# Performance work log

Hardware: AMD Instinct MI355X
Metric: run time of the kernel (lower is better)

## Reference

```python
import jax, jax.numpy as jnp
import numpy as np


def setup_inputs() -> dict:
    key = jax.random.key(0)
    ks = jax.random.split(key, 6)
    B, S, E, H = 8, 2048, 1024, 64
    scale = 1.0 / np.sqrt(E)
    return {
        "query": jax.random.normal(ks[0], (B, S, E), dtype=jnp.float32),
        "key": jax.random.normal(ks[1], (B, S, E), dtype=jnp.float32),
        "value": jax.random.normal(ks[2], (B, S, E), dtype=jnp.float32),
        "Wq": jax.random.normal(ks[3], (E, H), dtype=jnp.float32) * scale,
        "bq": jnp.zeros((H,), dtype=jnp.float32),
        "Wk": jax.random.normal(ks[4], (E, H), dtype=jnp.float32) * scale,
        "bk": jnp.zeros((H,), dtype=jnp.float32),
        "Wv": jax.random.normal(ks[5], (E, H), dtype=jnp.float32) * scale,
        "bv": jnp.zeros((H,), dtype=jnp.float32),
    }


def reference(query, key, value, Wq, bq, Wk, bk, Wv, bv):
    # Linear projections: [B,S,E] @ [E,H] + [H] -> [B,S,H]
    q = jnp.einsum("bse,eh->bsh", query, Wq) + bq
    k = jnp.einsum("bse,eh->bsh", key, Wk) + bk
    v = jnp.einsum("bse,eh->bsh", value, Wv) + bv
    head_dim = q.shape[-1]
    # scores [B,S,S], softmax over last axis, then weighted sum of values
    scores = jnp.einsum("bqh,bkh->bqk", q, k) / jnp.sqrt(
        jnp.asarray(head_dim, dtype=q.dtype)
    )
    attn = jax.nn.softmax(scores, axis=-1)
    return jnp.einsum("bqk,bkh->bqh", attn, v)
```

## Files before the change

### kernel.cpp

```cpp
#include <hip/hip_runtime.h>
#include <math.h>

#define BB 8
#define SS 2048
#define EE 1024
#define HH 64
#define MM (BB * SS)

typedef unsigned short u16;
typedef __attribute__((ext_vector_type(8))) short short8;
typedef __attribute__((ext_vector_type(4))) float floatx4;

__device__ __forceinline__ u16 f2bf(float f) {
    union { float f; unsigned u; } a; a.f = f;
    unsigned r = a.u + 0x7fffu + ((a.u >> 16) & 1u);
    return (u16)(r >> 16);
}

__device__ __forceinline__ void split2(float f0, float f1, unsigned& hp, unsigned& lp) {
    union { float f; unsigned u; } a0, a1, h0, h1, l0, l1;
    a0.f = f0; a1.f = f1;
    h0.u = a0.u & 0xffff0000u;
    h1.u = a1.u & 0xffff0000u;
    l0.f = f0 - h0.f;
    l1.f = f1 - h1.f;
    hp = __builtin_amdgcn_perm(a1.u, a0.u, 0x07060302u);
    lp = __builtin_amdgcn_perm(l1.u, l0.u, 0x07060302u);
}

__device__ __forceinline__ void async_copy16(const u16* g, u16* l) {
    __builtin_amdgcn_global_load_lds(
        (const __attribute__((address_space(1))) unsigned*)g,
        (__attribute__((address_space(3))) unsigned*)l, 16, 0, 0);
}

template <int CTRL>
__device__ __forceinline__ float dppf(float x) {
    union { float f; int i; } a, b;
    a.f = x;
    b.i = __builtin_amdgcn_update_dpp(a.i, a.i, CTRL, 0xF, 0xF, true);
    return b.f;
}
__device__ __forceinline__ float red_max16(float x) {
    x = fmaxf(x, dppf<0xB1>(x));
    x = fmaxf(x, dppf<0x4E>(x));
    x = fmaxf(x, dppf<0x141>(x));
    x = fmaxf(x, dppf<0x140>(x));
    return x;
}
__device__ __forceinline__ float red_sum16(float x) {
    x += dppf<0xB1>(x);
    x += dppf<0x4E>(x);
    x += dppf<0x141>(x);
    x += dppf<0x140>(x);
    return x;
}

#define WP_MAT 131072

__global__ __launch_bounds__(512) void pack_w(
    const float* __restrict__ W0, const float* __restrict__ W1, const float* __restrict__ W2,
    u16* __restrict__ Wp)
{
    const int which = blockIdx.y;
    const float* __restrict__ W = (which == 0) ? W0 : (which == 1) ? W1 : W2;
    const float scale = (which == 0) ? 0.125f : 1.0f;
    const int t    = blockIdx.x;
    const int tid  = threadIdx.x;
    const int ks   = tid >> 8;
    const int nt   = (tid >> 6) & 3;
    const int lane = tid & 63;
    const int n    = lane & 15;
    const int g    = lane >> 4;

    const int k0 = t * 64 + ks * 32 + g * 8;
    const int c  = nt * 16 + n;

    float e[8];
    #pragma unroll
    for (int j = 0; j < 8; ++j) e[j] = W[(size_t)(k0 + j) * HH + c] * scale;

    unsigned hp[4], lp[4];
    #pragma unroll
    for (int i = 0; i < 4; ++i) split2(e[2 * i], e[2 * i + 1], hp[i], lp[i]);

    u16* dst = Wp + (size_t)which * WP_MAT
                  + ((size_t)(t * 8 + ks * 4 + nt) * 2) * 512 + lane * 8;
    *(uint4*)dst         = (uint4){hp[0], hp[1], hp[2], hp[3]};
    *(uint4*)(dst + 512) = (uint4){lp[0], lp[1], lp[2], lp[3]};
}

#define PCH 16

#define LOAD_A(AV, T)                                   \
    {                                                   \
        const float* p_ = ap + (T) * 64;                \
        AV[0] = *(const float4*)(p_ + 0);               \
        AV[1] = *(const float4*)(p_ + 4);               \
        AV[2] = *(const float4*)(p_ + 32);              \
        AV[3] = *(const float4*)(p_ + 36);              \
    }

#define VBAR4()                                                     \
    {                                                               \
        __builtin_amdgcn_sched_barrier(0);                          \
        asm volatile("s_waitcnt vmcnt(4)" ::: "memory");            \
        __builtin_amdgcn_s_barrier();                               \
        __builtin_amdgcn_sched_barrier(0);                          \
    }

#define PROJ_CHUNK(AV, CURBUF, TSTAGE, TPREF)                                      \
    {                                                                              \
        if ((TSTAGE) < PCH) {                                                      \
            const u16* src_ = wpb + (size_t)(TSTAGE) * 8192 + wave * 2048 + lane * 8; \
            u16* dst_ = &Wb[(CURBUF) ^ 1][wave * 2048];                            \
            async_copy16(src_ + 0 * 512, dst_ + 0 * 512);                          \
            async_copy16(src_ + 1 * 512, dst_ + 1 * 512);                          \
            async_copy16(src_ + 2 * 512, dst_ + 2 * 512);                          \
            async_copy16(src_ + 3 * 512, dst_ + 3 * 512);                          \
        }                                                                          \
        __builtin_amdgcn_sched_barrier(0);                                         \
        short8 ah0, ah1, al0, al1;                                                 \
        {                                                                          \
            unsigned hp0, lp0, hp1, lp1, hp2, lp2, hp3, lp3;                       \
            split2(AV[0].x, AV[0].y, hp0, lp0);                                    \
            split2(AV[0].z, AV[0].w, hp1, lp1);                                    \
            split2(AV[1].x, AV[1].y, hp2, lp2);                                    \
            split2(AV[1].z, AV[1].w, hp3, lp3);                                    \
            union { uint4 u; short8 s; } ch_, cl_;                                 \
            ch_.u = (uint4){hp0, hp1, hp2, hp3};                                   \
            cl_.u = (uint4){lp0, lp1, lp2, lp3};                                   \
            ah0 = ch_.s; al0 = cl_.s;                                              \
            split2(AV[2].x, AV[2].y, hp0, lp0);                                    \
            split2(AV[2].z, AV[2].w, hp1, lp1);                                    \
            split2(AV[3].x, AV[3].y, hp2, lp2);                                    \
            split2(AV[3].z, AV[3].w, hp3, lp3);                                    \
            ch_.u = (uint4){hp0, hp1, hp2, hp3};                                   \
            cl_.u = (uint4){lp0, lp1, lp2, lp3};                                   \
            ah1 = ch_.s; al1 = cl_.s;                                              \
        }                                                                          \
        if ((TPREF) < PCH) LOAD_A(AV, TPREF);                                      \
        _Pragma("unroll")                                                          \
        for (int nt = 0; nt < 4; ++nt) {                                           \
            const short8 whf = *(const short8*)&Wb[CURBUF][nt * 1024 + lane * 8];  \
            const short8 wlf = *(const short8*)&Wb[CURBUF][nt * 1024 + 512 + lane * 8]; \
            acc[nt] = __builtin_amdgcn_mfma_f32_16x16x32_bf16(ah0, whf, acc[nt], 0, 0, 0); \
            acc[nt] = __builtin_amdgcn_mfma_f32_16x16x32_bf16(al0, whf, acc[nt], 0, 0, 0); \
            acc[nt] = __builtin_amdgcn_mfma_f32_16x16x32_bf16(ah0, wlf, acc[nt], 0, 0, 0); \
        }                                                                          \
        _Pragma("unroll")                                                          \
        for (int nt = 0; nt < 4; ++nt) {                                           \
            const short8 whf = *(const short8*)&Wb[CURBUF][4096 + nt * 1024 + lane * 8]; \
            const short8 wlf = *(const short8*)&Wb[CURBUF][4096 + nt * 1024 + 512 + lane * 8]; \
            acc[nt] = __builtin_amdgcn_mfma_f32_16x16x32_bf16(ah1, whf, acc[nt], 0, 0, 0); \
            acc[nt] = __builtin_amdgcn_mfma_f32_16x16x32_bf16(al1, whf, acc[nt], 0, 0, 0); \
            acc[nt] = __builtin_amdgcn_mfma_f32_16x16x32_bf16(ah1, wlf, acc[nt], 0, 0, 0); \
        }                                                                          \
    }

__global__ __launch_bounds__(256) void proj_mfma(
    const float* __restrict__ A0, const float* __restrict__ A1, const float* __restrict__ A2,
    const u16* __restrict__ Wp,
    const float* __restrict__ b0, const float* __restrict__ b1, const float* __restrict__ b2,
    u16* __restrict__ o0, u16* __restrict__ o1, u16* __restrict__ o2)
{
    const int which = blockIdx.y;
    const float* __restrict__ A    = (which == 0) ? A0 : (which == 1) ? A1 : A2;
    const float* __restrict__ bias = (which == 0) ? b0 : (which == 1) ? b1 : b2;
    u16* __restrict__ out          = (which == 0) ? o0 : (which == 1) ? o1 : o2;
    const float bscale = (which == 0) ? 0.125f : 1.0f;

    __shared__ __align__(16) u16 Wb[2][8192];

    const int tid  = threadIdx.x;
    const int lane = tid & 63;
    const int wave = tid >> 6;
    const int n    = lane & 15;
    const int g    = lane >> 4;
    const int row0 = blockIdx.x * 64;

    const float* __restrict__ ap = A + (size_t)(row0 + wave * 16 + n) * EE + g * 8;
    const u16* __restrict__ wpb = Wp + (size_t)which * WP_MAT;

    floatx4 acc[4];
    #pragma unroll
    for (int nt = 0; nt < 4; ++nt) acc[nt] = (floatx4){0.f, 0.f, 0.f, 0.f};

    float4 avA[4], avB[4];
    LOAD_A(avA, 0);
    LOAD_A(avB, 1);
    {
        const u16* src = wpb + wave * 2048 + lane * 8;
        u16* dst = &Wb[0][wave * 2048];
        #pragma unroll
        for (int i = 0; i < 4; ++i)
            async_copy16(src + i * 512, dst + i * 512);
    }
    __syncthreads();

    for (int tt = 0; tt < 12; tt += 2) {
        PROJ_CHUNK(avA, 0, tt + 1, tt + 2);
        VBAR4();
        PROJ_CHUNK(avB, 1, tt + 2, tt + 3);
        VBAR4();
    }
    PROJ_CHUNK(avA, 0, 13, 14);  VBAR4();
    PROJ_CHUNK(avB, 1, 14, 15);  VBAR4();
    PROJ_CHUNK(avA, 0, 15, 16);  __syncthreads();
    PROJ_CHUNK(avB, 1, 16, 17);

    #pragma unroll
    for (int nt = 0; nt < 4; ++nt) {
        const float bv = bias[nt * 16 + n] * bscale;
        #pragma unroll
        for (int r = 0; r < 4; ++r) {
            const int row = row0 + wave * 16 + g * 4 + r;
            out[(size_t)row * HH + nt * 16 + n] = f2bf(acc[nt][r] + bv);
        }
    }
}

__global__ __launch_bounds__(256) void flash_mfma(
    const u16* __restrict__ qp, const u16* __restrict__ kp,
    const u16* __restrict__ vp, float* __restrict__ out)
{
    __shared__ __align__(16) u16 Ks[2][64 * 64];
    __shared__ __align__(16) u16 Vt[2][64 * 64];
    __shared__ __align__(16) u16 Pw[4][16 * 72];

    const int b    = blockIdx.y;
    const int q0   = blockIdx.x * 32;
    const int tid  = threadIdx.x;
    const int lane = tid & 63;
    const int wave = tid >> 6;
    const int wq   = wave & 1;
    const int ks   = wave >> 1;
    const int n    = lane & 15;
    const int g    = lane >> 4;

    const u16* qrow = qp + ((size_t)b * SS + q0 + wq * 16 + n) * HH;
    const short8 qa0 = *(const short8*)(qrow + g * 8);
    const short8 qa1 = *(const short8*)(qrow + 32 + g * 8);

    floatx4 Oa[4];
    #pragma unroll
    for (int ht = 0; ht < 4; ++ht) Oa[ht] = (floatx4){0.f, 0.f, 0.f, 0.f};
    float m_i[4], l_ln[4];
    #pragma unroll
    for (int r = 0; r < 4; ++r) { m_i[r] = -1e30f; l_ln[r] = 0.f; }

    const u16* kb = kp + (size_t)b * SS * HH;
    const u16* vb = vp + (size_t)b * SS * HH;

    const int jK0 = tid >> 3, jK1 = 32 + (tid >> 3), cs = tid & 7;
    const int jV  = (tid & 15) * 4, hV = (tid >> 4) * 4;

    short8  kr0, kr1;
    ushort4 vr0, vr1, vr2, vr3;

    kr0 = *(const short8*)(kb + (size_t)jK0 * HH + cs * 8);
    kr1 = *(const short8*)(kb + (size_t)jK1 * HH + cs * 8);
    vr0 = *(const ushort4*)(vb + (size_t)(jV + 0) * HH + hV);
    vr1 = *(const ushort4*)(vb + (size_t)(jV + 1) * HH + hV);
    vr2 = *(const ushort4*)(vb + (size_t)(jV + 2) * HH + hV);
    vr3 = *(const ushort4*)(vb + (size_t)(jV + 3) * HH + hV);
    {
        *(short8*)&Ks[0][jK0 * 64 + ((cs ^ (jK0 & 7)) << 3)] = kr0;
        *(short8*)&Ks[0][jK1 * 64 + ((cs ^ (jK1 & 7)) << 3)] = kr1;
        const u16* a0 = (const u16*)&vr0; const u16* a1 = (const u16*)&vr1;
        const u16* a2 = (const u16*)&vr2; const u16* a3 = (const u16*)&vr3;
        #pragma unroll
        for (int i = 0; i < 4; ++i) {
            const int h = hV + i;
            ushort4 w; w.x = a0[i]; w.y = a1[i]; w.z = a2[i]; w.w = a3[i];
            *(ushort4*)((char*)&Vt[0][0] + h * 128 + (((jV >> 3) ^ (h & 7)) << 4) + ((jV & 4) << 1)) = w;
        }
    }
    __syncthreads();

    for (int t = 0; t < SS / 64; ++t) {
        const int cur = t & 1;

        if (t + 1 < SS / 64) {
            const size_t kt = (size_t)(t + 1) * 64;
            kr0 = *(const short8*)(kb + (kt + jK0) * HH + cs * 8);
            kr1 = *(const short8*)(kb + (kt + jK1) * HH + cs * 8);
            vr0 = *(const ushort4*)(vb + (kt + jV + 0) * HH + hV);
            vr1 = *(const ushort4*)(vb + (kt + jV + 1) * HH + hV);
            vr2 = *(const ushort4*)(vb + (kt + jV + 2) * HH + hV);
            vr3 = *(const ushort4*)(vb + (kt + jV + 3) * HH + hV);
        }

        floatx4 S[2];
        #pragma unroll
        for (int nt = 0; nt < 2; ++nt) {
            const int j = ks * 32 + nt * 16 + n;
            const short8 kf0 = *(const short8*)&Ks[cur][j * 64 + (((0 + g) ^ (j & 7)) << 3)];
            const short8 kf1 = *(const short8*)&Ks[cur][j * 64 + (((4 + g) ^ (j & 7)) << 3)];
            floatx4 a = (floatx4){0.f, 0.f, 0.f, 0.f};
            __builtin_amdgcn_s_setprio(1);
            a = __builtin_amdgcn_mfma_f32_16x16x32_bf16(qa0, kf0, a, 0, 0, 0);
            a = __builtin_amdgcn_mfma_f32_16x16x32_bf16(qa1, kf1, a, 0, 0, 0);
            __builtin_amdgcn_s_setprio(0);
            S[nt] = a;
        }

        float mx[4];
        #pragma unroll
        for (int r = 0; r < 4; ++r)
            mx[r] = red_max16(fmaxf(S[0][r], S[1][r]));

        float alpha[4];
        #pragma unroll
        for (int r = 0; r < 4; ++r) {
            const float Mn = fmaxf(m_i[r], mx[r]);
            alpha[r] = __expf(m_i[r] - Mn);
            m_i[r]   = Mn;
        }
        float p[2][4];
        #pragma unroll
        for (int nt = 0; nt < 2; ++nt)
            #pragma unroll
            for (int r = 0; r < 4; ++r)
                p[nt][r] = __expf(S[nt][r] - m_i[r]);
        #pragma unroll
        for (int r = 0; r < 4; ++r)
            l_ln[r] = l_ln[r] * alpha[r] + (p[0][r] + p[1][r]);
        #pragma unroll
        for (int ht = 0; ht < 4; ++ht)
            #pragma unroll
            for (int r = 0; r < 4; ++r) Oa[ht][r] *= alpha[r];

        #pragma unroll
        for (int nt = 0; nt < 2; ++nt)
            #pragma unroll
            for (int r = 0; r < 4; ++r)
                Pw[wave][(g * 4 + r) * 72 + nt * 16 + n] = f2bf(p[nt][r]);
        const short8 pa = *(const short8*)&Pw[wave][n * 72 + g * 8];

        __builtin_amdgcn_s_setprio(1);
        #pragma unroll
        for (int ht = 0; ht < 4; ++ht) {
            const int h = ht * 16 + n;
            const short8 vf = *(const short8*)((const char*)&Vt[cur][0] + h * 128 +
                                               ((((ks << 2) + g) ^ (h & 7)) << 4));
            Oa[ht] = __builtin_amdgcn_mfma_f32_16x16x32_bf16(pa, vf, Oa[ht], 0, 0, 0);
        }
        __builtin_amdgcn_s_setprio(0);

        if (t + 1 < SS / 64) {
            const int nx = cur ^ 1;
            *(short8*)&Ks[nx][jK0 * 64 + ((cs ^ (jK0 & 7)) << 3)] = kr0;
            *(short8*)&Ks[nx][jK1 * 64 + ((cs ^ (jK1 & 7)) << 3)] = kr1;
            const u16* a0 = (const u16*)&vr0; const u16* a1 = (const u16*)&vr1;
            const u16* a2 = (const u16*)&vr2; const u16* a3 = (const u16*)&vr3;
            #pragma unroll
            for (int i = 0; i < 4; ++i) {
                const int h = hV + i;
                ushort4 w; w.x = a0[i]; w.y = a1[i]; w.z = a2[i]; w.w = a3[i];
                *(ushort4*)((char*)&Vt[nx][0] + h * 128 + (((jV >> 3) ^ (h & 7)) << 4) + ((jV & 4) << 1)) = w;
            }
        }
        __syncthreads();
    }

    float l_i[4];
    #pragma unroll
    for (int r = 0; r < 4; ++r) l_i[r] = red_sum16(l_ln[r]);

    float* Cb = (float*)&Ks[0][0];
    float* Cm = Cb + 2 * 16 * 68;
    float* Cl = Cm + 32;
    if (ks == 1) {
        #pragma unroll
        for (int ht = 0; ht < 4; ++ht)
            #pragma unroll
            for (int r = 0; r < 4; ++r)
                Cb[(wq * 16 + g * 4 + r) * 68 + ht * 16 + n] = Oa[ht][r];
        if (n == 0)
            #pragma unroll
            for (int r = 0; r < 4; ++r) {
                Cm[wq * 16 + g * 4 + r] = m_i[r];
                Cl[wq * 16 + g * 4 + r] = l_i[r];
            }
    }
    __syncthreads();
    if (ks == 0) {
        float a0v[4], a1v[4], linv[4];
        #pragma unroll
        for (int r = 0; r < 4; ++r) {
            const int m = g * 4 + r;
            const float m1 = Cm[wq * 16 + m], l1 = Cl[wq * 16 + m];
            const float M  = fmaxf(m_i[r], m1);
            const float e0 = __expf(m_i[r] - M), e1 = __expf(m1 - M);
            a0v[r] = e0; a1v[r] = e1;
            linv[r] = 1.f / (l_i[r] * e0 + l1 * e1);
        }
        #pragma unroll
        for (int ht = 0; ht < 4; ++ht)
            #pragma unroll
            for (int r = 0; r < 4; ++r) {
                const float o1 = Cb[(wq * 16 + g * 4 + r) * 68 + ht * 16 + n];
                const float v  = (Oa[ht][r] * a0v[r] + o1 * a1v[r]) * linv[r];
                out[((size_t)b * SS + q0 + wq * 16 + g * 4 + r) * HH + ht * 16 + n] = v;
            }
    }
}

extern "C" void kernel_launch(void* const* d_in, const int* in_sizes, int n_in,
                              void* d_out, int out_size, void* d_ws, size_t ws_size,
                              hipStream_t stream) {
    const float* query = (const float*)d_in[0];
    const float* key   = (const float*)d_in[1];
    const float* value = (const float*)d_in[2];
    const float* Wq    = (const float*)d_in[3];
    const float* bq    = (const float*)d_in[4];
    const float* Wk    = (const float*)d_in[5];
    const float* bk    = (const float*)d_in[6];
    const float* Wv    = (const float*)d_in[7];
    const float* bv    = (const float*)d_in[8];
    float* out = (float*)d_out;

    u16* qp = (u16*)d_ws;
    u16* kp = qp + (size_t)MM * HH;
    u16* vp = kp + (size_t)MM * HH;
    u16* Wp = vp + (size_t)MM * HH;

    dim3 wgrid(EE / 64, 3);
    pack_w<<<wgrid, 512, 0, stream>>>(Wq, Wk, Wv, Wp);

    dim3 pgrid(MM / 64, 3);
    proj_mfma<<<pgrid, 256, 0, stream>>>(query, key, value,
                                         Wp,
                                         bq, bk, bv,
                                         qp, kp, vp);

    dim3 agrid(SS / 32, BB);
    flash_mfma<<<agrid, 256, 0, stream>>>(qp, kp, vp, out);
}
```

Baseline: 260.0 us.

## Widen flash block to 8 waves over 128-key tiles with single-buffered LDS

The attention kernel now runs 512 threads per block and processes 128 keys per iteration, splitting the key dimension across four wave groups instead of two. The shared K/V tiles become single-buffered, with an extra barrier before writing the next tile. The final merge combines four partial softmax states per query row instead of two. The aim is more parallel work per block and fewer loop iterations. The cost is that the double-buffer overlap is lost, an extra sync is added per iteration, and the merge epilogue is heavier.

Result: no change. 261.5 us (+0.6%).

```diff
diff --git a/kernel.cpp b/kernel.cpp
--- a/kernel.cpp
+++ b/kernel.cpp
@@ -220,13 +220,43 @@
     }
 }
 
-__global__ __launch_bounds__(256) void flash_mfma(
+#define KVB 128
+#define NIT (SS / KVB)
+
+#define WRITE_KV()                                                              \
+    {                                                                           \
+        *(short8*)&Ks[jK * 64 + ((cs2 ^ (jK & 7)) << 3)]       = kr0;           \
+        *(short8*)&Ks[jK * 64 + (((cs2 + 1) ^ (jK & 7)) << 3)] = kr1;           \
+        const u16* a0 = (const u16*)&vr0; const u16* a1 = (const u16*)&vr1;     \
+        const u16* a2 = (const u16*)&vr2; const u16* a3 = (const u16*)&vr3;     \
+        _Pragma("unroll")                                                       \
+        for (int i = 0; i < 4; ++i) {                                           \
+            const int h = hV + i;                                               \
+            ushort4 w; w.x = a0[i]; w.y = a1[i]; w.z = a2[i]; w.w = a3[i];      \
+            *(ushort4*)((char*)Vt + h * 256 + (((jV >> 3) ^ (h & 7)) << 4)      \
+                        + ((jV & 4) << 1)) = w;                                 \
+        }                                                                       \
+    }
+
+#define LOAD_KV(T)                                                              \
+    {                                                                           \
+        const size_t kt = (size_t)(T) * KVB;                                    \
+        kr0 = *(const short8*)(kb + (kt + jK) * HH + cs2 * 8);                  \
+        kr1 = *(const short8*)(kb + (kt + jK) * HH + cs2 * 8 + 8);              \
+        vr0 = *(const ushort4*)(vb + (kt + jV + 0) * HH + hV);                  \
+        vr1 = *(const ushort4*)(vb + (kt + jV + 1) * HH + hV);                  \
+        vr2 = *(const ushort4*)(vb + (kt + jV + 2) * HH + hV);                  \
+        vr3 = *(const ushort4*)(vb + (kt + jV + 3) * HH + hV);                  \
+    }
+
+__global__ __launch_bounds__(512) void flash_mfma(
     const u16* __restrict__ qp, const u16* __restrict__ kp,
     const u16* __restrict__ vp, float* __restrict__ out)
 {
-    __shared__ __align__(16) u16 Ks[2][64 * 64];
-    __shared__ __align__(16) u16 Vt[2][64 * 64];
-    __shared__ __align__(16) u16 Pw[4][16 * 72];
+    __shared__ __align__(16) u16 SM[25600];
+    u16* Ks = SM;
+    u16* Vt = SM + 8192;
+    u16* Pw = SM + 16384;
 
     const int b    = blockIdx.y;
     const int q0   = blockIdx.x * 32;
@@ -252,51 +282,27 @@
     const u16* kb = kp + (size_t)b * SS * HH;
     const u16* vb = vp + (size_t)b * SS * HH;
 
-    const int jK0 = tid >> 3, jK1 = 32 + (tid >> 3), cs = tid & 7;
-    const int jV  = (tid & 15) * 4, hV = (tid >> 4) * 4;
+    const int jK  = tid >> 2;
+    const int cs2 = (tid & 3) * 2;
+    const int jV  = (tid & 31) * 4;
+    const int hV  = (tid >> 5) * 4;
 
     short8  kr0, kr1;
     ushort4 vr0, vr1, vr2, vr3;
 
-    kr0 = *(const short8*)(kb + (size_t)jK0 * HH + cs * 8);
-    kr1 = *(const short8*)(kb + (size_t)jK1 * HH + cs * 8);
-    vr0 = *(const ushort4*)(vb + (size_t)(jV + 0) * HH + hV);
-    vr1 = *(const ushort4*)(vb + (size_t)(jV + 1) * HH + hV);
-    vr2 = *(const ushort4*)(vb + (size_t)(jV + 2) * HH + hV);
-    vr3 = *(const ushort4*)(vb + (size_t)(jV + 3) * HH + hV);
-    {
-        *(short8*)&Ks[0][jK0 * 64 + ((cs ^ (jK0 & 7)) << 3)] = kr0;
-        *(short8*)&Ks[0][jK1 * 64 + ((cs ^ (jK1 & 7)) << 3)] = kr1;
-        const u16* a0 = (const u16*)&vr0; const u16* a1 = (const u16*)&vr1;
-        const u16* a2 = (const u16*)&vr2; const u16* a3 = (const u16*)&vr3;
-        #pragma unroll
-        for (int i = 0; i < 4; ++i) {
-            const int h = hV + i;
-            ushort4 w; w.x = a0[i]; w.y = a1[i]; w.z = a2[i]; w.w = a3[i];
-            *(ushort4*)((char*)&Vt[0][0] + h * 128 + (((jV >> 3) ^ (h & 7)) << 4) + ((jV & 4) << 1)) = w;
-        }
-    }
+    LOAD_KV(0);
+    WRITE_KV();
     __syncthreads();
 
-    for (int t = 0; t < SS / 64; ++t) {
-        const int cur = t & 1;
-
-        if (t + 1 < SS / 64) {
-            const size_t kt = (size_t)(t + 1) * 64;
-            kr0 = *(const short8*)(kb + (kt + jK0) * HH + cs * 8);
-            kr1 = *(const short8*)(kb + (kt + jK1) * HH + cs * 8);
-            vr0 = *(const ushort4*)(vb + (kt + jV + 0) * HH + hV);
-            vr1 = *(const ushort4*)(vb + (kt + jV + 1) * HH + hV);
-            vr2 = *(const ushort4*)(vb + (kt + jV + 2) * HH + hV);
-            vr3 = *(const ushort4*)(vb + (kt + jV + 3) * HH + hV);
-        }
+    for (int t = 0; t < NIT; ++t) {
+        if (t + 1 < NIT) LOAD_KV(t + 1);
 
         floatx4 S[2];
         #pragma unroll
         for (int nt = 0; nt < 2; ++nt) {
             const int j = ks * 32 + nt * 16 + n;
-            const short8 kf0 = *(const short8*)&Ks[cur][j * 64 + (((0 + g) ^ (j & 7)) << 3)];
-            const short8 kf1 = *(const short8*)&Ks[cur][j * 64 + (((4 + g) ^ (j & 7)) << 3)];
+            const short8 kf0 = *(const short8*)&Ks[j * 64 + (((0 + g) ^ (j & 7)) << 3)];
+            const short8 kf1 = *(const short8*)&Ks[j * 64 + (((4 + g) ^ (j & 7)) << 3)];
             floatx4 a = (floatx4){0.f, 0.f, 0.f, 0.f};
             __builtin_amdgcn_s_setprio(1);
             a = __builtin_amdgcn_mfma_f32_16x16x32_bf16(qa0, kf0, a, 0, 0, 0);
@@ -335,74 +341,75 @@
         for (int nt = 0; nt < 2; ++nt)
             #pragma unroll
             for (int r = 0; r < 4; ++r)
-                Pw[wave][(g * 4 + r) * 72 + nt * 16 + n] = f2bf(p[nt][r]);
-        const short8 pa = *(const short8*)&Pw[wave][n * 72 + g * 8];
+                Pw[wave * 1152 + (g * 4 + r) * 72 + nt * 16 + n] = f2bf(p[nt][r]);
+        const short8 pa = *(const short8*)&Pw[wave * 1152 + n * 72 + g * 8];
 
         __builtin_amdgcn_s_setprio(1);
         #pragma unroll
         for (int ht = 0; ht < 4; ++ht) {
             const int h = ht * 16 + n;
-            const short8 vf = *(const short8*)((const char*)&Vt[cur][0] + h * 128 +
+            const short8 vf = *(const short8*)((const char*)Vt + h * 256 +
                                                ((((ks << 2) + g) ^ (h & 7)) << 4));
             Oa[ht] = __builtin_amdgcn_mfma_f32_16x16x32_bf16(pa, vf, Oa[ht], 0, 0, 0);
         }
         __builtin_amdgcn_s_setprio(0);
 
-        if (t + 1 < SS / 64) {
-            const int nx = cur ^ 1;
-            *(short8*)&Ks[nx][jK0 * 64 + ((cs ^ (jK0 & 7)) << 3)] = kr0;
-            *(short8*)&Ks[nx][jK1 * 64 + ((cs ^ (jK1 & 7)) << 3)] = kr1;
-            const u16* a0 = (const u16*)&vr0; const u16* a1 = (const u16*)&vr1;
-            const u16* a2 = (const u16*)&vr2; const u16* a3 = (const u16*)&vr3;
-            #pragma unroll
-            for (int i = 0; i < 4; ++i) {
-                const int h = hV + i;
-                ushort4 w; w.x = a0[i]; w.y = a1[i]; w.z = a2[i]; w.w = a3[i];
-                *(ushort4*)((char*)&Vt[nx][0] + h * 128 + (((jV >> 3) ^ (h & 7)) << 4) + ((jV & 4) << 1)) = w;
-            }
-        }
         __syncthreads();
+        if (t + 1 < NIT) WRITE_KV();
+        __syncthreads();
     }
 
     float l_i[4];
     #pragma unroll
     for (int r = 0; r < 4; ++r) l_i[r] = red_sum16(l_ln[r]);
 
-    float* Cb = (float*)&Ks[0][0];
-    float* Cm = Cb + 2 * 16 * 68;
-    float* Cl = Cm + 32;
-    if (ks == 1) {
+    float* Cb = (float*)SM;
+    float* Cm = Cb + 3 * 2 * 16 * 68;
+    float* Cl = Cm + 96;
+
+    if (ks != 0) {
+        float* dst = Cb + ((ks - 1) * 2 + wq) * 16 * 68;
         #pragma unroll
         for (int ht = 0; ht < 4; ++ht)
             #pragma unroll
             for (int r = 0; r < 4; ++r)
-                Cb[(wq * 16 + g * 4 + r) * 68 + ht * 16 + n] = Oa[ht][r];
+                dst[(g * 4 + r) * 68 + ht * 16 + n] = Oa[ht][r];
         if (n == 0)
             #pragma unroll
             for (int r = 0; r < 4; ++r) {
-                Cm[wq * 16 + g * 4 + r] = m_i[r];
-                Cl[wq * 16 + g * 4 + r] = l_i[r];
+                Cm[((ks - 1) * 2 + wq) * 16 + g * 4 + r] = m_i[r];
+                Cl[((ks - 1) * 2 + wq) * 16 + g * 4 + r] = l_i[r];
             }
     }
     __syncthreads();
     if (ks == 0) {
-        float a0v[4], a1v[4], linv[4];
+        float e0[4], e1[4], e2[4], e3[4], linv[4];
         #pragma unroll
         for (int r = 0; r < 4; ++r) {
             const int m = g * 4 + r;
-            const float m1 = Cm[wq * 16 + m], l1 = Cl[wq * 16 + m];
-            const float M  = fmaxf(m_i[r], m1);
-            const float e0 = __expf(m_i[r] - M), e1 = __expf(m1 - M);
-            a0v[r] = e0; a1v[r] = e1;
-            linv[r] = 1.f / (l_i[r] * e0 + l1 * e1);
+            const float m1 = Cm[(0 * 2 + wq) * 16 + m];
+            const float m2 = Cm[(1 * 2 + wq) * 16 + m];
+            const float m3 = Cm[(2 * 2 + wq) * 16 + m];
+            const float l1 = Cl[(0 * 2 + wq) * 16 + m];
+            const float l2 = Cl[(1 * 2 + wq) * 16 + m];
+            const float l3 = Cl[(2 * 2 + wq) * 16 + m];
+            float M = fmaxf(fmaxf(m_i[r], m1), fmaxf(m2, m3));
+            e0[r] = __expf(m_i[r] - M);
+            e1[r] = __expf(m1 - M);
+            e2[r] = __expf(m2 - M);
+            e3[r] = __expf(m3 - M);
+            linv[r] = 1.f / (l_i[r] * e0[r] + l1 * e1[r] + l2 * e2[r] + l3 * e3[r]);
         }
         #pragma unroll
         for (int ht = 0; ht < 4; ++ht)
             #pragma unroll
             for (int r = 0; r < 4; ++r) {
-                const float o1 = Cb[(wq * 16 + g * 4 + r) * 68 + ht * 16 + n];
-                const float v  = (Oa[ht][r] * a0v[r] + o1 * a1v[r]) * linv[r];
-                out[((size_t)b * SS + q0 + wq * 16 + g * 4 + r) * HH + ht * 16 + n] = v;
+                const int m = g * 4 + r;
+                const float o1 = Cb[((0 * 2 + wq) * 16 + m) * 68 + ht * 16 + n];
+                const float o2 = Cb[((1 * 2 + wq) * 16 + m) * 68 + ht * 16 + n];
+                const float o3 = Cb[((2 * 2 + wq) * 16 + m) * 68 + ht * 16 + n];
+                const float v  = (Oa[ht][r] * e0[r] + o1 * e1[r] + o2 * e2[r] + o3 * e3[r]) * linv[r];
+                out[((size_t)b * SS + q0 + wq * 16 + m) * HH + ht * 16 + n] = v;
             }
     }
 }
@@ -436,5 +443,5 @@
                                          qp, kp, vp);
 
     dim3 agrid(SS / 32, BB);
-    flash_mfma<<<agrid, 256, 0, stream>>>(qp, kp, vp, out);
-}
+    flash_mfma<<<agrid, 512, 0, stream>>>(qp, kp, vp, out);
+}
```

## Split projection output columns across wave pairs with 512-thread blocks

Applied to the files above, without the earlier changes.

The projection kernel now launches 8 waves per block instead of 4. Each pair of waves shares one 16-row group and splits the 64 output columns into two halves, so each wave holds half as many accumulators and issues half the MFMAs per chunk. Weight staging into LDS is spread over all 8 waves. In exchange, both waves of a pair load and split the same A rows, which doubles global A reads and the hi/lo conversion work per block.

After: 259.1 us. No clear change (-0.3%).

```diff
diff --git a/kernel.cpp b/kernel.cpp
--- a/kernel.cpp
+++ b/kernel.cpp
@@ -112,12 +112,10 @@
 #define PROJ_CHUNK(AV, CURBUF, TSTAGE, TPREF)                                      \
     {                                                                              \
         if ((TSTAGE) < PCH) {                                                      \
-            const u16* src_ = wpb + (size_t)(TSTAGE) * 8192 + wave * 2048 + lane * 8; \
-            u16* dst_ = &Wb[(CURBUF) ^ 1][wave * 2048];                            \
-            async_copy16(src_ + 0 * 512, dst_ + 0 * 512);                          \
-            async_copy16(src_ + 1 * 512, dst_ + 1 * 512);                          \
-            async_copy16(src_ + 2 * 512, dst_ + 2 * 512);                          \
-            async_copy16(src_ + 3 * 512, dst_ + 3 * 512);                          \
+            const u16* src_ = wpb + (size_t)(TSTAGE) * 8192 + wave * 512 + lane * 8; \
+            u16* dst_ = &Wb[(CURBUF) ^ 1][wave * 512];                             \
+            async_copy16(src_,        dst_);                                       \
+            async_copy16(src_ + 4096, dst_ + 4096);                                \
         }                                                                          \
         __builtin_amdgcn_sched_barrier(0);                                         \
         short8 ah0, ah1, al0, al1;                                                 \
@@ -141,24 +139,26 @@
         }                                                                          \
         if ((TPREF) < PCH) LOAD_A(AV, TPREF);                                      \
         _Pragma("unroll")                                                          \
-        for (int nt = 0; nt < 4; ++nt) {                                           \
-            const short8 whf = *(const short8*)&Wb[CURBUF][nt * 1024 + lane * 8];  \
-            const short8 wlf = *(const short8*)&Wb[CURBUF][nt * 1024 + 512 + lane * 8]; \
-            acc[nt] = __builtin_amdgcn_mfma_f32_16x16x32_bf16(ah0, whf, acc[nt], 0, 0, 0); \
-            acc[nt] = __builtin_amdgcn_mfma_f32_16x16x32_bf16(al0, whf, acc[nt], 0, 0, 0); \
-            acc[nt] = __builtin_amdgcn_mfma_f32_16x16x32_bf16(ah0, wlf, acc[nt], 0, 0, 0); \
+        for (int nt2 = 0; nt2 < 2; ++nt2) {                                        \
+            const int f0 = (0 * 4 + nh * 2 + nt2) * 1024;                          \
+            const short8 whf = *(const short8*)&Wb[CURBUF][f0 + lane * 8];         \
+            const short8 wlf = *(const short8*)&Wb[CURBUF][f0 + 512 + lane * 8];   \
+            acc[nt2] = __builtin_amdgcn_mfma_f32_16x16x32_bf16(ah0, whf, acc[nt2], 0, 0, 0); \
+            acc[nt2] = __builtin_amdgcn_mfma_f32_16x16x32_bf16(al0, whf, acc[nt2], 0, 0, 0); \
+            acc[nt2] = __builtin_amdgcn_mfma_f32_16x16x32_bf16(ah0, wlf, acc[nt2], 0, 0, 0); \
         }                                                                          \
         _Pragma("unroll")                                                          \
-        for (int nt = 0; nt < 4; ++nt) {                                           \
-            const short8 whf = *(const short8*)&Wb[CURBUF][4096 + nt * 1024 + lane * 8]; \
-            const short8 wlf = *(const short8*)&Wb[CURBUF][4096 + nt * 1024 + 512 + lane * 8]; \
-            acc[nt] = __builtin_amdgcn_mfma_f32_16x16x32_bf16(ah1, whf, acc[nt], 0, 0, 0); \
-            acc[nt] = __builtin_amdgcn_mfma_f32_16x16x32_bf16(al1, whf, acc[nt], 0, 0, 0); \
-            acc[nt] = __builtin_amdgcn_mfma_f32_16x16x32_bf16(ah1, wlf, acc[nt], 0, 0, 0); \
+        for (int nt2 = 0; nt2 < 2; ++nt2) {                                        \
+            const int f1 = (1 * 4 + nh * 2 + nt2) * 1024;                          \
+            const short8 whf = *(const short8*)&Wb[CURBUF][f1 + lane * 8];         \
+            const short8 wlf = *(const short8*)&Wb[CURBUF][f1 + 512 + lane * 8];   \
+            acc[nt2] = __builtin_amdgcn_mfma_f32_16x16x32_bf16(ah1, whf, acc[nt2], 0, 0, 0); \
+            acc[nt2] = __builtin_amdgcn_mfma_f32_16x16x32_bf16(al1, whf, acc[nt2], 0, 0, 0); \
+            acc[nt2] = __builtin_amdgcn_mfma_f32_16x16x32_bf16(ah1, wlf, acc[nt2], 0, 0, 0); \
         }                                                                          \
     }
 
-__global__ __launch_bounds__(256) void proj_mfma(
+__global__ __launch_bounds__(512) void proj_mfma(
     const float* __restrict__ A0, const float* __restrict__ A1, const float* __restrict__ A2,
     const u16* __restrict__ Wp,
     const float* __restrict__ b0, const float* __restrict__ b1, const float* __restrict__ b2,
@@ -175,26 +175,27 @@
     const int tid  = threadIdx.x;
     const int lane = tid & 63;
     const int wave = tid >> 6;
+    const int rg   = wave >> 1;
+    const int nh   = wave & 1;
     const int n    = lane & 15;
     const int g    = lane >> 4;
     const int row0 = blockIdx.x * 64;
 
-    const float* __restrict__ ap = A + (size_t)(row0 + wave * 16 + n) * EE + g * 8;
+    const float* __restrict__ ap = A + (size_t)(row0 + rg * 16 + n) * EE + g * 8;
     const u16* __restrict__ wpb = Wp + (size_t)which * WP_MAT;
 
-    floatx4 acc[4];
-    #pragma unroll
-    for (int nt = 0; nt < 4; ++nt) acc[nt] = (floatx4){0.f, 0.f, 0.f, 0.f};
+    floatx4 acc[2];
+    acc[0] = (floatx4){0.f, 0.f, 0.f, 0.f};
+    acc[1] = (floatx4){0.f, 0.f, 0.f, 0.f};
 
     float4 avA[4], avB[4];
     LOAD_A(avA, 0);
     LOAD_A(avB, 1);
     {
-        const u16* src = wpb + wave * 2048 + lane * 8;
-        u16* dst = &Wb[0][wave * 2048];
-        #pragma unroll
-        for (int i = 0; i < 4; ++i)
-            async_copy16(src + i * 512, dst + i * 512);
+        const u16* src = wpb + wave * 512 + lane * 8;
+        u16* dst = &Wb[0][wave * 512];
+        async_copy16(src,        dst);
+        async_copy16(src + 4096, dst + 4096);
     }
     __syncthreads();
 
@@ -210,12 +211,13 @@
     PROJ_CHUNK(avB, 1, 16, 17);
 
     #pragma unroll
-    for (int nt = 0; nt < 4; ++nt) {
-        const float bv = bias[nt * 16 + n] * bscale;
+    for (int nt2 = 0; nt2 < 2; ++nt2) {
+        const int col = nh * 32 + nt2 * 16 + n;
+        const float bv = bias[col] * bscale;
         #pragma unroll
         for (int r = 0; r < 4; ++r) {
-            const int row = row0 + wave * 16 + g * 4 + r;
-            out[(size_t)row * HH + nt * 16 + n] = f2bf(acc[nt][r] + bv);
+            const int row = row0 + rg * 16 + g * 4 + r;
+            out[(size_t)row * HH + col] = f2bf(acc[nt2][r] + bv);
         }
     }
 }
@@ -430,7 +432,7 @@
     pack_w<<<wgrid, 512, 0, stream>>>(Wq, Wk, Wv, Wp);
 
     dim3 pgrid(MM / 64, 3);
-    proj_mfma<<<pgrid, 256, 0, stream>>>(query, key, value,
+    proj_mfma<<<pgrid, 512, 0, stream>>>(query, key, value,
                                          Wp,
                                          bq, bk, bv,
                                          qp, kp, vp);
```

## Triple-buffer weight staging and deepen A-prefetch in projection kernel

Applied to the files above, without the earlier changes.

The projection kernel moves from double to triple buffering of the weight tiles in shared memory. It adds a third register set so A rows are prefetched three chunks ahead, and it retunes the vmcnt waits to keep more global loads in flight across barriers. The goal is to hide global-load latency in the projection stage, at the cost of more LDS and registers, which may lower occupancy.

Measured after the change: 258.0 us (median of 2 runs). No clear change (-0.8%).

```diff
diff --git a/kernel.cpp b/kernel.cpp
--- a/kernel.cpp
+++ b/kernel.cpp
@@ -101,24 +101,27 @@
         AV[3] = *(const float4*)(p_ + 36);              \
     }
 
-#define VBAR4()                                                     \
+#define STAGE_W(TSTAGE, SBUF)                                                  \
+    {                                                                          \
+        const u16* src_ = wpb + (size_t)(TSTAGE) * 8192 + wave * 2048 + lane * 8; \
+        u16* dst_ = &Wb[SBUF][wave * 2048];                                    \
+        async_copy16(src_ + 0 * 512, dst_ + 0 * 512);                          \
+        async_copy16(src_ + 1 * 512, dst_ + 1 * 512);                          \
+        async_copy16(src_ + 2 * 512, dst_ + 2 * 512);                          \
+        async_copy16(src_ + 3 * 512, dst_ + 3 * 512);                          \
+    }
+
+#define VBARN(N)                                                    \
     {                                                               \
         __builtin_amdgcn_sched_barrier(0);                          \
-        asm volatile("s_waitcnt vmcnt(4)" ::: "memory");            \
+        asm volatile("s_waitcnt vmcnt(" #N ")" ::: "memory");       \
         __builtin_amdgcn_s_barrier();                               \
         __builtin_amdgcn_sched_barrier(0);                          \
     }
 
-#define PROJ_CHUNK(AV, CURBUF, TSTAGE, TPREF)                                      \
+#define PROJ_CHUNK(AV, WBUF, SBUF, TSTAGE, TPREF)                                  \
     {                                                                              \
-        if ((TSTAGE) < PCH) {                                                      \
-            const u16* src_ = wpb + (size_t)(TSTAGE) * 8192 + wave * 2048 + lane * 8; \
-            u16* dst_ = &Wb[(CURBUF) ^ 1][wave * 2048];                            \
-            async_copy16(src_ + 0 * 512, dst_ + 0 * 512);                          \
-            async_copy16(src_ + 1 * 512, dst_ + 1 * 512);                          \
-            async_copy16(src_ + 2 * 512, dst_ + 2 * 512);                          \
-            async_copy16(src_ + 3 * 512, dst_ + 3 * 512);                          \
-        }                                                                          \
+        if ((TSTAGE) < PCH) STAGE_W(TSTAGE, SBUF);                                 \
         __builtin_amdgcn_sched_barrier(0);                                         \
         short8 ah0, ah1, al0, al1;                                                 \
         {                                                                          \
@@ -142,16 +145,16 @@
         if ((TPREF) < PCH) LOAD_A(AV, TPREF);                                      \
         _Pragma("unroll")                                                          \
         for (int nt = 0; nt < 4; ++nt) {                                           \
-            const short8 whf = *(const short8*)&Wb[CURBUF][nt * 1024 + lane * 8];  \
-            const short8 wlf = *(const short8*)&Wb[CURBUF][nt * 1024 + 512 + lane * 8]; \
+            const short8 whf = *(const short8*)&Wb[WBUF][nt * 1024 + lane * 8];    \
+            const short8 wlf = *(const short8*)&Wb[WBUF][nt * 1024 + 512 + lane * 8]; \
             acc[nt] = __builtin_amdgcn_mfma_f32_16x16x32_bf16(ah0, whf, acc[nt], 0, 0, 0); \
             acc[nt] = __builtin_amdgcn_mfma_f32_16x16x32_bf16(al0, whf, acc[nt], 0, 0, 0); \
             acc[nt] = __builtin_amdgcn_mfma_f32_16x16x32_bf16(ah0, wlf, acc[nt], 0, 0, 0); \
         }                                                                          \
         _Pragma("unroll")                                                          \
         for (int nt = 0; nt < 4; ++nt) {                                           \
-            const short8 whf = *(const short8*)&Wb[CURBUF][4096 + nt * 1024 + lane * 8]; \
-            const short8 wlf = *(const short8*)&Wb[CURBUF][4096 + nt * 1024 + 512 + lane * 8]; \
+            const short8 whf = *(const short8*)&Wb[WBUF][4096 + nt * 1024 + lane * 8]; \
+            const short8 wlf = *(const short8*)&Wb[WBUF][4096 + nt * 1024 + 512 + lane * 8]; \
             acc[nt] = __builtin_amdgcn_mfma_f32_16x16x32_bf16(ah1, whf, acc[nt], 0, 0, 0); \
             acc[nt] = __builtin_amdgcn_mfma_f32_16x16x32_bf16(al1, whf, acc[nt], 0, 0, 0); \
             acc[nt] = __builtin_amdgcn_mfma_f32_16x16x32_bf16(ah1, wlf, acc[nt], 0, 0, 0); \
@@ -170,7 +173,7 @@
     u16* __restrict__ out          = (which == 0) ? o0 : (which == 1) ? o1 : o2;
     const float bscale = (which == 0) ? 0.125f : 1.0f;
 
-    __shared__ __align__(16) u16 Wb[2][8192];
+    __shared__ __align__(16) u16 Wb[3][8192];
 
     const int tid  = threadIdx.x;
     const int lane = tid & 63;
@@ -186,28 +189,30 @@
     #pragma unroll
     for (int nt = 0; nt < 4; ++nt) acc[nt] = (floatx4){0.f, 0.f, 0.f, 0.f};
 
-    float4 avA[4], avB[4];
+    float4 avA[4], avB[4], avC[4];
+    STAGE_W(0, 0);
+    __builtin_amdgcn_sched_barrier(0);
     LOAD_A(avA, 0);
     LOAD_A(avB, 1);
-    {
-        const u16* src = wpb + wave * 2048 + lane * 8;
-        u16* dst = &Wb[0][wave * 2048];
-        #pragma unroll
-        for (int i = 0; i < 4; ++i)
-            async_copy16(src + i * 512, dst + i * 512);
-    }
-    __syncthreads();
-
-    for (int tt = 0; tt < 12; tt += 2) {
-        PROJ_CHUNK(avA, 0, tt + 1, tt + 2);
-        VBAR4();
-        PROJ_CHUNK(avB, 1, tt + 2, tt + 3);
-        VBAR4();
-    }
-    PROJ_CHUNK(avA, 0, 13, 14);  VBAR4();
-    PROJ_CHUNK(avB, 1, 14, 15);  VBAR4();
-    PROJ_CHUNK(avA, 0, 15, 16);  __syncthreads();
-    PROJ_CHUNK(avB, 1, 16, 17);
+    LOAD_A(avC, 2);
+    __builtin_amdgcn_sched_barrier(0);
+    STAGE_W(1, 1);
+    VBARN(12);
+
+    PROJ_CHUNK(avA, 0, 2, 2, 3);
+    VBARN(8);
+
+    for (int tt = 1; tt <= 10; tt += 3) {
+        PROJ_CHUNK(avB, 1, 0, tt + 2, tt + 3);  VBARN(12);
+        PROJ_CHUNK(avC, 2, 1, tt + 3, tt + 4);  VBARN(12);
+        PROJ_CHUNK(avA, 0, 2, tt + 4, tt + 5);  VBARN(12);
+    }
+
+    PROJ_CHUNK(avB, 1, 0, 15, 16);
+    VBARN(8);
+    PROJ_CHUNK(avC, 2, 0, 16, 17);
+    VBARN(0);
+    PROJ_CHUNK(avA, 0, 0, 16, 17);
 
     #pragma unroll
     for (int nt = 0; nt < 4; ++nt) {
```
